# Performance work log

Hardware: AMD Instinct MI355X
Metric: run time of the kernel (lower is better)

## Reference

```python
import jax, jax.numpy as jnp
import numpy as np

GAMMA = 0.001

N_TEST, N_TRAIN, D, OUT = 8192, 8192, 512, 16

def setup_inputs() -> dict:
    key = jax.random.key(0)
    k1, k2, k3 = jax.random.split(key, 3)
    X = jax.random.normal(k1, (N_TEST, D), dtype=jnp.float32)
    train_X = jax.random.normal(k2, (N_TRAIN, D), dtype=jnp.float32)
    alpha = jax.random.normal(k3, (N_TRAIN, OUT), dtype=jnp.float32)
    return {"X": X, "train_X": train_X, "alpha": alpha}


def reference(X, train_X, alpha):
    # (same math as (x[:,None]-y[None])**2 summed over d, without the n*m*d blowup)
    x_sq = jnp.sum(X * X, axis=-1, keepdims=True)            # [n_test, 1]
    y_sq = jnp.sum(train_X * train_X, axis=-1)[None, :]       # [1, n_train]
    cross = X @ train_X.T                                     # [n_test, n_train]
    sq = x_sq + y_sq - 2.0 * cross
    K_test = jnp.exp(-GAMMA * sq)
    return K_test @ alpha                                     # [n_test, out]
```

## Files before the change

kernel.cpp:

```cpp
#include <hip/hip_runtime.h>
#include <stdint.h>

#define NROW 8192
#define DIM  512
#define NOUT 16
#define GAMMA 0.001f
#define EXP2S (2.0f * GAMMA * 1.44269504088896340736f)
#define SC1 0x7F7F7F7F

typedef __bf16 bf16_t;
typedef bf16_t bf16x4_t __attribute__((ext_vector_type(4)));
typedef bf16_t bf16x8_t __attribute__((ext_vector_type(8)));
typedef float  floatx4_t __attribute__((ext_vector_type(4)));
typedef int    intx4_t  __attribute__((ext_vector_type(4)));
typedef int    intx8_t  __attribute__((ext_vector_type(8)));

__device__ __forceinline__ void async_copy16(const void* g, const void* l) {
    __builtin_amdgcn_global_load_lds(
        (__attribute__((address_space(1))) void*)(uintptr_t)g,
        (__attribute__((address_space(3))) void*)(uint32_t)(uintptr_t)l,
        16, 0, 0);
}

__global__ __launch_bounds__(256) void prep_convert(
    const float* __restrict__ X, const float* __restrict__ T,
    const float* __restrict__ alpha,
    uint8_t* __restrict__ Xf, uint8_t* __restrict__ Tf,
    float* __restrict__ xfac, bf16_t* __restrict__ alphaTp)
{
    const int w = threadIdx.x >> 6, lane = threadIdx.x & 63;
    const int row = blockIdx.x * 4 + w;
    const bool is_test = row < NROW;
    const float* src = is_test ? X : T;
    uint8_t* dst = is_test ? Xf : Tf;
    const int r = is_test ? row : row - NROW;
    const float4* s4 = (const float4*)(src + (size_t)r * DIM);
    const float4 v0 = s4[lane * 2];
    const float4 v1 = s4[lane * 2 + 1];
    float ss = v0.x*v0.x + v0.y*v0.y + v0.z*v0.z + v0.w*v0.w
             + v1.x*v1.x + v1.y*v1.y + v1.z*v1.z + v1.w*v1.w;
    int lo = __builtin_amdgcn_cvt_pk_fp8_f32(v0.x, v0.y, 0, false);
    lo     = __builtin_amdgcn_cvt_pk_fp8_f32(v0.z, v0.w, lo, true);
    int hi = __builtin_amdgcn_cvt_pk_fp8_f32(v1.x, v1.y, 0, false);
    hi     = __builtin_amdgcn_cvt_pk_fp8_f32(v1.z, v1.w, hi, true);
    *(int2*)(dst + (size_t)r * DIM + lane * 8) = make_int2(lo, hi);
#pragma unroll
    for (int m = 32; m > 0; m >>= 1) ss += __shfl_xor(ss, m, 64);
    const float f = __expf(-GAMMA * ss);
    if (is_test) {
        if (lane == 0) xfac[r] = f;
    } else if (lane < 16) {
        alphaTp[(size_t)lane * NROW + r] = (bf16_t)(alpha[r * 16 + lane] * f);
    }
}

#define TPT 4
#define KLD2 72

__global__ __launch_bounds__(256, 2) void rbf_main(
    const uint8_t* __restrict__ Xf, const uint8_t* __restrict__ Tf,
    const bf16_t* __restrict__ alphaTp, const float* __restrict__ xfac,
    float* __restrict__ out)
{
    __shared__ __align__(16) unsigned char smem[4 * 64 * KLD2 * 2];

    const int tid = threadIdx.x;
    const int w = tid >> 6, lane = tid & 63;
    const int wm = w >> 1, wn = w & 1;
    const int quad = lane >> 4, l15 = lane & 15;

    const int rb = blockIdx.x;
    const int chunk = blockIdx.y;
    const int row0 = rb * 128;
    const int cb0 = chunk * (TPT * 128);

    const int s_row = tid >> 3;
    const int s_ub = (((tid & 7) ^ (s_row & 7)) * 16);
    const uint8_t* gXp = Xf + (size_t)(row0 + s_row) * DIM + s_ub;
    const uint8_t* gTp = Tf + (size_t)(cb0 + s_row) * DIM + s_ub;
    const unsigned ldsW = (unsigned)(w << 10);

    const int sw = l15 & 7;
    const int ub0 = ((2 * quad) ^ sw) * 16;
    const int ub1 = ((2 * quad + 1) ^ sw) * 16;

    intx8_t xr[4][4];
#pragma unroll
    for (int i = 0; i < 4; ++i)
        async_copy16(gXp + (size_t)i * 16384, smem + i * 4096 + ldsW);
#pragma unroll
    for (int g = 0; g < 4; ++g) {
        __syncthreads();
        if (g < 3) {
            const unsigned bb = ((g + 1) & 1) * 16384u;
#pragma unroll
            for (int i = 0; i < 4; ++i)
                async_copy16(gXp + (size_t)i * 16384 + (g + 1) * 128,
                             smem + bb + i * 4096 + ldsW);
        }
        const unsigned char* bufc = smem + (g & 1) * 16384;
#pragma unroll
        for (int ni = 0; ni < 4; ++ni) {
            const int rB = wn * 64 + ni * 16 + l15;
            const intx4_t blo = *(const intx4_t*)(bufc + rB * 128 + ub0);
            const intx4_t bhi = *(const intx4_t*)(bufc + rB * 128 + ub1);
            xr[g][ni] = __builtin_shufflevector(blo, bhi, 0, 1, 2, 3, 4, 5, 6, 7);
        }
    }

    const floatx4_t vzero = {0.f, 0.f, 0.f, 0.f};
    floatx4_t oacc[4];
#pragma unroll
    for (int i = 0; i < 4; ++i) oacc[i] = vzero;

    bf16_t* kw = (bf16_t*)smem + w * (64 * KLD2);

    for (int t = 0; t < TPT; ++t) {
        const int cb = cb0 + t * 128;
        const uint8_t* gTt = gTp + (size_t)t * 128 * DIM;

        floatx4_t acc[4][4];
#pragma unroll
        for (int i = 0; i < 4; ++i)
#pragma unroll
            for (int j = 0; j < 4; ++j) acc[i][j] = vzero;

        __syncthreads();
#pragma unroll
        for (int i = 0; i < 4; ++i)
            async_copy16(gTt + (size_t)i * 16384, smem + i * 4096 + ldsW);

#pragma unroll
        for (int g = 0; g < 4; ++g) {
            __syncthreads();
            if (g < 3) {
                const unsigned bb = ((g + 1) & 1) * 16384u;
                const int kb = (g + 1) * 128;
#pragma unroll
                for (int i = 0; i < 4; ++i)
                    async_copy16(gTt + (size_t)i * 16384 + kb,
                                 smem + bb + i * 4096 + ldsW);
            }
            const unsigned char* bufc = smem + (g & 1) * 16384;
#pragma unroll
            for (int mi = 0; mi < 4; ++mi) {
                const int rA = wm * 64 + mi * 16 + l15;
                const intx4_t alo = *(const intx4_t*)(bufc + rA * 128 + ub0);
                const intx4_t ahi = *(const intx4_t*)(bufc + rA * 128 + ub1);
                const intx8_t ta = __builtin_shufflevector(alo, ahi, 0, 1, 2, 3, 4, 5, 6, 7);
#pragma unroll
                for (int ni = 0; ni < 4; ++ni)
                    acc[mi][ni] = __builtin_amdgcn_mfma_scale_f32_16x16x128_f8f6f4(
                        ta, xr[g][ni], acc[mi][ni], 0, 0, 0, SC1, 0, SC1);
            }
        }

        __syncthreads();
#pragma unroll
        for (int ni = 0; ni < 4; ++ni)
#pragma unroll
            for (int mi = 0; mi < 4; ++mi) {
                bf16x4_t pk;
#pragma unroll
                for (int r = 0; r < 4; ++r)
                    pk[r] = (bf16_t)__builtin_amdgcn_exp2f(acc[mi][ni][r] * EXP2S);
                *(bf16x4_t*)(kw + (ni * 16 + l15) * KLD2 + mi * 16 + quad * 4) = pk;
            }

#pragma unroll
        for (int ks = 0; ks < 2; ++ks) {
            const bf16x8_t bv = *(const bf16x8_t*)(alphaTp + (size_t)l15 * NROW
                                                   + cb + wm * 64 + ks * 32 + quad * 8);
#pragma unroll
            for (int ni = 0; ni < 4; ++ni) {
                const bf16x8_t av = *(const bf16x8_t*)(kw + (ni * 16 + l15) * KLD2
                                                       + ks * 32 + quad * 8);
                oacc[ni] = __builtin_amdgcn_mfma_f32_16x16x32_bf16(av, bv, oacc[ni], 0, 0, 0);
            }
        }
    }

    __syncthreads();
    float* stash = (float*)smem;
    if (wm == 1) {
#pragma unroll
        for (int ni = 0; ni < 4; ++ni)
            *(floatx4_t*)(stash + wn * 1024 + ni * 256 + lane * 4) = oacc[ni];
    }
    __syncthreads();
    if (wm == 0) {
#pragma unroll
        for (int ni = 0; ni < 4; ++ni) {
            const floatx4_t o2 = *(const floatx4_t*)(stash + wn * 1024 + ni * 256 + lane * 4);
            const int trow = row0 + wn * 64 + ni * 16 + quad * 4;
            const float4 xf = *(const float4*)(xfac + trow);
            atomicAdd(out + (size_t)(trow + 0) * NOUT + l15, (oacc[ni][0] + o2[0]) * xf.x);
            atomicAdd(out + (size_t)(trow + 1) * NOUT + l15, (oacc[ni][1] + o2[1]) * xf.y);
            atomicAdd(out + (size_t)(trow + 2) * NOUT + l15, (oacc[ni][2] + o2[2]) * xf.z);
            atomicAdd(out + (size_t)(trow + 3) * NOUT + l15, (oacc[ni][3] + o2[3]) * xf.w);
        }
    }
}

extern "C" void kernel_launch(void* const* d_in, const int* in_sizes, int n_in,
                              void* d_out, int out_size, void* d_ws, size_t ws_size,
                              hipStream_t stream) {
    (void)in_sizes; (void)n_in; (void)out_size; (void)ws_size;
    const float* X     = (const float*)d_in[0];
    const float* T     = (const float*)d_in[1];
    const float* alpha = (const float*)d_in[2];

    char* ws = (char*)d_ws;
    uint8_t* Xf     = (uint8_t*)ws;
    uint8_t* Tf     = (uint8_t*)(ws + (8u << 20));
    float*   xfac   = (float*)(ws + (16u << 20));
    bf16_t*  alphaTp= (bf16_t*)(ws + (16u << 20) + (64u << 10));
    float*   out    = (float*)d_out;

    hipMemsetAsync(out, 0, (size_t)NROW * NOUT * sizeof(float), stream);
    prep_convert<<<4096, 256, 0, stream>>>(X, T, alpha, Xf, Tf, xfac, alphaTp);
    dim3 grid(64, 16);
    rbf_main<<<grid, 256, 0, stream>>>(Xf, Tf, alphaTp, xfac, out);
}
```

Baseline: 133.2 us.

## Prepack test rows in MFMA fragment order and stream them from global

The prep kernel now writes the FP8 test matrix in a fragment-native layout so each lane can load its MFMA B-operand directly from global memory with two 16-byte loads. The main kernel no longer preloads all 16 X fragments through LDS into registers. Instead it streams the current k-group fragments with a one-step register prefetch inside the train-tile loop. This frees registers (16 intx8 down to 8) and removes the upfront LDS staging phase, at the cost of re-reading X from global or L2 for every train tile.

```diff
diff --git a/kernel.cpp b/kernel.cpp
--- a/kernel.cpp
+++ b/kernel.cpp
@@ -22,17 +22,22 @@
         16, 0, 0);
 }
 
+__device__ __forceinline__ intx8_t ld_frag(const uint8_t* p) {
+    const intx4_t lo = *(const intx4_t*)(p);
+    const intx4_t hi = *(const intx4_t*)(p + 16);
+    return __builtin_shufflevector(lo, hi, 0, 1, 2, 3, 4, 5, 6, 7);
+}
+
 __global__ __launch_bounds__(256) void prep_convert(
     const float* __restrict__ X, const float* __restrict__ T,
     const float* __restrict__ alpha,
-    uint8_t* __restrict__ Xf, uint8_t* __restrict__ Tf,
+    uint8_t* __restrict__ X2, uint8_t* __restrict__ Tf,
     float* __restrict__ xfac, bf16_t* __restrict__ alphaTp)
 {
     const int w = threadIdx.x >> 6, lane = threadIdx.x & 63;
     const int row = blockIdx.x * 4 + w;
     const bool is_test = row < NROW;
     const float* src = is_test ? X : T;
-    uint8_t* dst = is_test ? Xf : Tf;
     const int r = is_test ? row : row - NROW;
     const float4* s4 = (const float4*)(src + (size_t)r * DIM);
     const float4 v0 = s4[lane * 2];
@@ -43,7 +48,14 @@
     lo     = __builtin_amdgcn_cvt_pk_fp8_f32(v0.z, v0.w, lo, true);
     int hi = __builtin_amdgcn_cvt_pk_fp8_f32(v1.x, v1.y, 0, false);
     hi     = __builtin_amdgcn_cvt_pk_fp8_f32(v1.z, v1.w, hi, true);
-    *(int2*)(dst + (size_t)r * DIM + lane * 8) = make_int2(lo, hi);
+    if (is_test) {
+        const size_t off = ((size_t)(((r >> 4) << 2) + (lane >> 4)) << 11)
+                         + (size_t)((((lane >> 2) & 3) * 16 + (r & 15)) * 32
+                                    + (lane & 3) * 8);
+        *(int2*)(X2 + off) = make_int2(lo, hi);
+    } else {
+        *(int2*)(Tf + (size_t)r * DIM + lane * 8) = make_int2(lo, hi);
+    }
 #pragma unroll
     for (int m = 32; m > 0; m >>= 1) ss += __shfl_xor(ss, m, 64);
     const float f = __expf(-GAMMA * ss);
@@ -58,7 +70,7 @@
 #define KLD2 72
 
 __global__ __launch_bounds__(256, 2) void rbf_main(
-    const uint8_t* __restrict__ Xf, const uint8_t* __restrict__ Tf,
+    const uint8_t* __restrict__ X2, const uint8_t* __restrict__ Tf,
     const bf16_t* __restrict__ alphaTp, const float* __restrict__ xfac,
     float* __restrict__ out)
 {
@@ -76,7 +88,6 @@
 
     const int s_row = tid >> 3;
     const int s_ub = (((tid & 7) ^ (s_row & 7)) * 16);
-    const uint8_t* gXp = Xf + (size_t)(row0 + s_row) * DIM + s_ub;
     const uint8_t* gTp = Tf + (size_t)(cb0 + s_row) * DIM + s_ub;
     const unsigned ldsW = (unsigned)(w << 10);
 
@@ -84,29 +95,10 @@
     const int ub0 = ((2 * quad) ^ sw) * 16;
     const int ub1 = ((2 * quad + 1) ^ sw) * 16;
 
-    intx8_t xr[4][4];
-#pragma unroll
-    for (int i = 0; i < 4; ++i)
-        async_copy16(gXp + (size_t)i * 16384, smem + i * 4096 + ldsW);
-#pragma unroll
-    for (int g = 0; g < 4; ++g) {
-        __syncthreads();
-        if (g < 3) {
-            const unsigned bb = ((g + 1) & 1) * 16384u;
-#pragma unroll
-            for (int i = 0; i < 4; ++i)
-                async_copy16(gXp + (size_t)i * 16384 + (g + 1) * 128,
-                             smem + bb + i * 4096 + ldsW);
-        }
-        const unsigned char* bufc = smem + (g & 1) * 16384;
-#pragma unroll
-        for (int ni = 0; ni < 4; ++ni) {
-            const int rB = wn * 64 + ni * 16 + l15;
-            const intx4_t blo = *(const intx4_t*)(bufc + rB * 128 + ub0);
-            const intx4_t bhi = *(const intx4_t*)(bufc + rB * 128 + ub1);
-            xr[g][ni] = __builtin_shufflevector(blo, bhi, 0, 1, 2, 3, 4, 5, 6, 7);
-        }
-    }
+    const uint8_t* xg[4];
+#pragma unroll
+    for (int ni = 0; ni < 4; ++ni)
+        xg[ni] = X2 + (((size_t)((rb * 8 + wn * 4 + ni) * 4)) << 11) + lane * 32;
 
     const floatx4_t vzero = {0.f, 0.f, 0.f, 0.f};
     floatx4_t oacc[4];
@@ -114,6 +106,10 @@
     for (int i = 0; i < 4; ++i) oacc[i] = vzero;
 
     bf16_t* kw = (bf16_t*)smem + w * (64 * KLD2);
+
+    intx8_t xc[4], xn[4];
+#pragma unroll
+    for (int ni = 0; ni < 4; ++ni) xc[ni] = ld_frag(xg[ni]);
 
     for (int t = 0; t < TPT; ++t) {
         const int cb = cb0 + t * 128;
@@ -140,6 +136,13 @@
                 for (int i = 0; i < 4; ++i)
                     async_copy16(gTt + (size_t)i * 16384 + kb,
                                  smem + bb + i * 4096 + ldsW);
+#pragma unroll
+                for (int ni = 0; ni < 4; ++ni)
+                    xn[ni] = ld_frag(xg[ni] + ((g + 1) << 11));
+            } else if (t + 1 < TPT) {
+#pragma unroll
+                for (int ni = 0; ni < 4; ++ni)
+                    xn[ni] = ld_frag(xg[ni]);
             }
             const unsigned char* bufc = smem + (g & 1) * 16384;
 #pragma unroll
@@ -151,8 +154,10 @@
 #pragma unroll
                 for (int ni = 0; ni < 4; ++ni)
                     acc[mi][ni] = __builtin_amdgcn_mfma_scale_f32_16x16x128_f8f6f4(
-                        ta, xr[g][ni], acc[mi][ni], 0, 0, 0, SC1, 0, SC1);
-            }
+                        ta, xc[ni], acc[mi][ni], 0, 0, 0, SC1, 0, SC1);
+            }
+#pragma unroll
+            for (int ni = 0; ni < 4; ++ni) xc[ni] = xn[ni];
         }
 
         __syncthreads();
@@ -211,14 +216,14 @@
     const float* alpha = (const float*)d_in[2];
 
     char* ws = (char*)d_ws;
-    uint8_t* Xf     = (uint8_t*)ws;
+    uint8_t* X2     = (uint8_t*)ws;
     uint8_t* Tf     = (uint8_t*)(ws + (8u << 20));
     float*   xfac   = (float*)(ws + (16u << 20));
     bf16_t*  alphaTp= (bf16_t*)(ws + (16u << 20) + (64u << 10));
     float*   out    = (float*)d_out;
 
     hipMemsetAsync(out, 0, (size_t)NROW * NOUT * sizeof(float), stream);
-    prep_convert<<<4096, 256, 0, stream>>>(X, T, alpha, Xf, Tf, xfac, alphaTp);
+    prep_convert<<<4096, 256, 0, stream>>>(X, T, alpha, X2, Tf, xfac, alphaTp);
     dim3 grid(64, 16);
-    rbf_main<<<grid, 256, 0, stream>>>(Xf, Tf, alphaTp, xfac, out);
-}
+    rbf_main<<<grid, 256, 0, stream>>>(X2, Tf, alphaTp, xfac, out);
+}
```

Result: no change. 134.1 us (+0.7%).
